# Optimization experiments

Hardware: AMD Instinct MI355X
Metric: run time of the kernel (lower is better)

## Reference

```python
import jax, jax.numpy as jnp
import numpy as np

jax.config.update("jax_enable_x64", True)  # anchor_ids * 2654435761 needs int64, matching torch semantics

B, NV, D = 200000, 5, 64
CANTOR_DEPTH = 8
VOLUME_SCALE = 10.0
VOLUME_W, EDGE_W, SPREAD_W = 0.4, 0.3, 0.3
EPS = 1e-6
KNUTH = 2654435761


def setup_inputs() -> dict:
    key = jax.random.key(0)
    vertices = jax.random.normal(key, (B, NV, D), dtype=jnp.float32)
    anchor_ids = jnp.arange(B, dtype=jnp.int64)
    return {"vertices": vertices, "anchor_ids": anchor_ids}


def reference(vertices, anchor_ids):
    dtype = vertices.dtype
    b = vertices.shape[0]

    # pairwise squared distances between the 5 vertices: [B, 5, 5]
    diff = vertices[:, :, None, :] - vertices[:, None, :, :]
    dist_sq = (diff ** 2).sum(-1)

    # Cayley-Menger 6x6 matrix and 4-simplex volume
    M = jnp.zeros((b, 6, 6), dtype=dtype)
    M = M.at[:, 0, 1:].set(1.0)
    M = M.at[:, 1:, 0].set(1.0)
    M = M.at[:, 1:, 1:].set(dist_sq)
    det = jnp.linalg.det(M)
    volume = jnp.sqrt(jnp.clip(-det / 9216.0, 0.0))

    # edge statistics over the 10 unique edges (unbiased std, as torch.std)
    iu, ju = np.triu_indices(5, k=1)
    edges = jnp.sqrt(dist_sq[:, iu, ju])  # [B, 10]
    mean_edge = edges.mean(axis=1)
    std_edge = edges.std(axis=1, ddof=1)

    # vertex spread: std of distances to centroid (unbiased)
    centroid = vertices.mean(axis=1, keepdims=True)
    dists = jnp.linalg.norm(vertices - centroid, axis=-1)  # [B, 5]
    spread = dists.std(axis=1, ddof=1)

    volume_norm = jax.nn.sigmoid(volume * VOLUME_SCALE)
    edge_ratio = jax.nn.sigmoid(std_edge / (mean_edge + EPS))
    spread_norm = jax.nn.sigmoid(spread)
    seed = volume_norm * VOLUME_W + edge_ratio * EDGE_W + spread_norm * SPREAD_W

    # anchor id hash contribution (int64 modular arithmetic as in torch)
    id_contrib = ((anchor_ids.astype(jnp.int64) * KNUTH) % 1000000).astype(dtype) / 1000000.0
    seed = 0.1 * seed + 0.9 * id_contrib
    seed = jnp.clip(seed, EPS, 1.0 - EPS)

    # Cantor digit extraction (unrolled fixed-depth loop)
    x = seed
    cantor_val = jnp.zeros_like(x)
    factor = 0.5
    for _ in range(CANTOR_DEPTH):
        x_scaled = x * 3.0
        digit = x_scaled.astype(jnp.int32)  # trunc == floor for x >= 0
        x = x_scaled - digit.astype(dtype)
        cantor_val = cantor_val + (digit == 2).astype(dtype) * factor
        factor *= 0.5
    return jnp.clip(cantor_val, 0.0, 1.0)
```

## Files before the change

### kernel.cpp

```cpp
#include <hip/hip_runtime.h>
#include <stdint.h>


#define THREADS 256
#define ANCH_PER_BLOCK 256

__global__ __launch_bounds__(THREADS) void fingerprint_kernel(
    const float* __restrict__ vertices,
    const void* __restrict__ ids_raw,
    float* __restrict__ out,
    int n)
{
    __shared__ double stats[ANCH_PER_BLOCK][17];

    const int tid  = threadIdx.x;
    const int wave = tid >> 6;
    const int lane = tid & 63;
    const int g    = lane >> 4;
    const int r    = lane & 15;
    const int blockBase = blockIdx.x * ANCH_PER_BLOCK;

    const int PI[10] = {0,0,0,0,1,1,1,2,2,3};
    const int PJ[10] = {1,2,3,4,2,3,4,3,4,4};

    #pragma unroll 1
    for (int it = 0; it < ANCH_PER_BLOCK / (4 * 4); ++it) {
        const int alocal = wave * 64 + it * 4 + g;
        int a = blockBase + alocal;
        int aload = (a < n) ? a : (n - 1);

        const float4* vp = (const float4*)(vertices + (size_t)aload * 320);
        float xv[5][4];
        #pragma unroll
        for (int v = 0; v < 5; ++v) {
            float4 t = vp[v * 16 + r];
            xv[v][0] = t.x; xv[v][1] = t.y; xv[v][2] = t.z; xv[v][3] = t.w;
        }

        double ds[10], sd[5];
        #pragma unroll
        for (int p = 0; p < 10; ++p) ds[p] = 0.0;
        #pragma unroll
        for (int v = 0; v < 5; ++v) sd[v] = 0.0;

        #pragma unroll
        for (int k = 0; k < 4; ++k) {
            double x0 = (double)xv[0][k], x1 = (double)xv[1][k],
                   x2 = (double)xv[2][k], x3 = (double)xv[3][k],
                   x4 = (double)xv[4][k];
            double c = (x0 + x1 + x2 + x3 + x4) * 0.2;
            double d0 = x0 - c, d1 = x1 - c, d2 = x2 - c, d3 = x3 - c, d4 = x4 - c;
            sd[0] += d0 * d0; sd[1] += d1 * d1; sd[2] += d2 * d2;
            sd[3] += d3 * d3; sd[4] += d4 * d4;
            double xs[5] = {x0, x1, x2, x3, x4};
            #pragma unroll
            for (int p = 0; p < 10; ++p) {
                double dd = xs[PI[p]] - xs[PJ[p]];
                ds[p] += dd * dd;
            }
        }

        #pragma unroll
        for (int p = 0; p < 10; ++p) {
            ds[p] += __shfl_xor(ds[p], 1);
            ds[p] += __shfl_xor(ds[p], 2);
            ds[p] += __shfl_xor(ds[p], 4);
            ds[p] += __shfl_xor(ds[p], 8);
        }
        #pragma unroll
        for (int v = 0; v < 5; ++v) {
            sd[v] += __shfl_xor(sd[v], 1);
            sd[v] += __shfl_xor(sd[v], 2);
            sd[v] += __shfl_xor(sd[v], 4);
            sd[v] += __shfl_xor(sd[v], 8);
        }

        if (r < 10)       stats[alocal][r]      = ds[r];
        else if (r < 15)  stats[alocal][r]      = sd[r - 10];
    }

    __syncthreads();

    const int a = blockBase + tid;
    if (a >= n) return;

    double ds[10], sd[5];
    #pragma unroll
    for (int p = 0; p < 10; ++p) ds[p] = stats[tid][p];
    #pragma unroll
    for (int v = 0; v < 5; ++v) sd[v] = stats[tid][10 + v];

    const int PIDX[5][5] = {
        {-1, 0, 1, 2, 3},
        { 0,-1, 4, 5, 6},
        { 1, 4,-1, 7, 8},
        { 2, 5, 7,-1, 9},
        { 3, 6, 8, 9,-1}};

    double M[6][6];
    M[0][0] = 0.0;
    #pragma unroll
    for (int j = 1; j < 6; ++j) { M[0][j] = 1.0; M[j][0] = 1.0; }
    #pragma unroll
    for (int i = 0; i < 5; ++i)
        #pragma unroll
        for (int j = 0; j < 5; ++j)
            M[1 + i][1 + j] = (i == j) ? 0.0 : ds[PIDX[i][j]];

    double sign = 1.0;
    #pragma unroll
    for (int k = 0; k < 6; ++k) {
        #pragma unroll
        for (int i = k + 1; i < 6; ++i) {
            bool sw = fabs(M[i][k]) > fabs(M[k][k]);
            #pragma unroll
            for (int j = 0; j < 6; ++j) {
                double tk = M[k][j], ti = M[i][j];
                M[k][j] = sw ? ti : tk;
                M[i][j] = sw ? tk : ti;
            }
            sign = sw ? -sign : sign;
        }
        double rp = 1.0 / M[k][k];
        #pragma unroll
        for (int i = k + 1; i < 6; ++i) {
            double l = M[i][k] * rp;
            #pragma unroll
            for (int j = k + 1; j < 6; ++j)
                M[i][j] -= l * M[k][j];
        }
    }
    double det = sign;
    #pragma unroll
    for (int k = 0; k < 6; ++k) det *= M[k][k];

    double volume = sqrt(fmax(-det / 9216.0, 0.0));

    double e[10], esum = 0.0;
    #pragma unroll
    for (int p = 0; p < 10; ++p) { e[p] = sqrt(ds[p]); esum += e[p]; }
    double emean = esum * 0.1;
    double evar = 0.0;
    #pragma unroll
    for (int p = 0; p < 10; ++p) { double d = e[p] - emean; evar += d * d; }
    double estd = sqrt(evar / 9.0);

    double dd[5], dsum = 0.0;
    #pragma unroll
    for (int v = 0; v < 5; ++v) { dd[v] = sqrt(sd[v]); dsum += dd[v]; }
    double dmean = dsum * 0.2;
    double svar = 0.0;
    #pragma unroll
    for (int v = 0; v < 5; ++v) { double d = dd[v] - dmean; svar += d * d; }
    double spread = sqrt(svar * 0.25);

    double vn = 1.0 / (1.0 + exp(-10.0 * volume));
    double er = 1.0 / (1.0 + exp(-(estd / (emean + 1e-6))));
    double sn = 1.0 / (1.0 + exp(-spread));
    double seed = 0.4 * vn + 0.3 * er + 0.3 * sn;

    const int* ai32 = (const int*)ids_raw;
    long long idv;
    if (ai32[1] == 0) {
        idv = ((const long long*)ids_raw)[a];
    } else {
        idv = (long long)ai32[a];
    }
    long long h = (idv * 2654435761LL) % 1000000LL;
    double idc = (double)h / 1000000.0;

    seed = 0.1 * seed + 0.9 * idc;
    seed = fmin(fmax(seed, 1e-6), 1.0 - 1e-6);

    double x = seed, cant = 0.0, factor = 0.5;
    #pragma unroll
    for (int itc = 0; itc < 8; ++itc) {
        double xs = x * 3.0;
        int dg = (int)xs;
        x = xs - (double)dg;
        cant += (dg == 2) ? factor : 0.0;
        factor *= 0.5;
    }
    out[a] = (float)fmin(fmax(cant, 0.0), 1.0);
}

extern "C" void kernel_launch(void* const* d_in, const int* in_sizes, int n_in,
                              void* d_out, int out_size, void* d_ws, size_t ws_size,
                              hipStream_t stream) {
    const float* vertices = (const float*)d_in[0];
    const void*  ids      = d_in[1];
    float* out = (float*)d_out;
    int n = in_sizes[1];
    int grid = (n + ANCH_PER_BLOCK - 1) / ANCH_PER_BLOCK;
    fingerprint_kernel<<<grid, THREADS, 0, stream>>>(vertices, ids, out, n);
}
```

Measured before the change: 379.9 us.

## Compute Gram inner products and replace Cayley-Menger LU with Gram determinant

Phase one now accumulates the 15 pairwise inner products per anchor in fp64, using 8 lanes per anchor with two float4 loads each. Pairwise distances, centroid distances and a 4x4 Gram matrix are derived from these products, and the volume comes from a closed-form Gram determinant instead of a pivoted 6x6 LU. This trims FP64 work, shuffle rounds and the heavy elimination code. It risks cancellation error when distances are recovered from inner products.

```diff
diff --git a/kernel.cpp b/kernel.cpp
--- a/kernel.cpp
+++ b/kernel.cpp
@@ -16,67 +16,67 @@
     const int tid  = threadIdx.x;
     const int wave = tid >> 6;
     const int lane = tid & 63;
-    const int g    = lane >> 4;
-    const int r    = lane & 15;
+    const int g    = lane >> 3;
+    const int r    = lane & 7;
     const int blockBase = blockIdx.x * ANCH_PER_BLOCK;
 
-    const int PI[10] = {0,0,0,0,1,1,1,2,2,3};
-    const int PJ[10] = {1,2,3,4,2,3,4,3,4,4};
-
-    #pragma unroll 1
-    for (int it = 0; it < ANCH_PER_BLOCK / (4 * 4); ++it) {
-        const int alocal = wave * 64 + it * 4 + g;
+    #pragma unroll 2
+    for (int it = 0; it < 8; ++it) {
+        const int alocal = wave * 64 + it * 8 + g;
         int a = blockBase + alocal;
         int aload = (a < n) ? a : (n - 1);
 
         const float4* vp = (const float4*)(vertices + (size_t)aload * 320);
-        float xv[5][4];
+        float xa[5][4], xb[5][4];
         #pragma unroll
         for (int v = 0; v < 5; ++v) {
             float4 t = vp[v * 16 + r];
-            xv[v][0] = t.x; xv[v][1] = t.y; xv[v][2] = t.z; xv[v][3] = t.w;
-        }
-
-        double ds[10], sd[5];
-        #pragma unroll
-        for (int p = 0; p < 10; ++p) ds[p] = 0.0;
-        #pragma unroll
-        for (int v = 0; v < 5; ++v) sd[v] = 0.0;
+            xa[v][0] = t.x; xa[v][1] = t.y; xa[v][2] = t.z; xa[v][3] = t.w;
+        }
+        #pragma unroll
+        for (int v = 0; v < 5; ++v) {
+            float4 t = vp[v * 16 + 8 + r];
+            xb[v][0] = t.x; xb[v][1] = t.y; xb[v][2] = t.z; xb[v][3] = t.w;
+        }
+
+        double ip[15];
+        #pragma unroll
+        for (int p = 0; p < 15; ++p) ip[p] = 0.0;
 
         #pragma unroll
         for (int k = 0; k < 4; ++k) {
-            double x0 = (double)xv[0][k], x1 = (double)xv[1][k],
-                   x2 = (double)xv[2][k], x3 = (double)xv[3][k],
-                   x4 = (double)xv[4][k];
-            double c = (x0 + x1 + x2 + x3 + x4) * 0.2;
-            double d0 = x0 - c, d1 = x1 - c, d2 = x2 - c, d3 = x3 - c, d4 = x4 - c;
-            sd[0] += d0 * d0; sd[1] += d1 * d1; sd[2] += d2 * d2;
-            sd[3] += d3 * d3; sd[4] += d4 * d4;
-            double xs[5] = {x0, x1, x2, x3, x4};
-            #pragma unroll
-            for (int p = 0; p < 10; ++p) {
-                double dd = xs[PI[p]] - xs[PJ[p]];
-                ds[p] += dd * dd;
-            }
-        }
-
-        #pragma unroll
-        for (int p = 0; p < 10; ++p) {
-            ds[p] += __shfl_xor(ds[p], 1);
-            ds[p] += __shfl_xor(ds[p], 2);
-            ds[p] += __shfl_xor(ds[p], 4);
-            ds[p] += __shfl_xor(ds[p], 8);
-        }
-        #pragma unroll
-        for (int v = 0; v < 5; ++v) {
-            sd[v] += __shfl_xor(sd[v], 1);
-            sd[v] += __shfl_xor(sd[v], 2);
-            sd[v] += __shfl_xor(sd[v], 4);
-            sd[v] += __shfl_xor(sd[v], 8);
-        }
-
-        if (r < 10)       stats[alocal][r]      = ds[r];
-        else if (r < 15)  stats[alocal][r]      = sd[r - 10];
+            double x[5];
+            #pragma unroll
+            for (int v = 0; v < 5; ++v) x[v] = (double)xa[v][k];
+            int p = 0;
+            #pragma unroll
+            for (int v = 0; v < 5; ++v)
+                #pragma unroll
+                for (int w = v; w < 5; ++w)
+                    ip[p++] = fma(x[v], x[w], ip[p]);
+        }
+        #pragma unroll
+        for (int k = 0; k < 4; ++k) {
+            double x[5];
+            #pragma unroll
+            for (int v = 0; v < 5; ++v) x[v] = (double)xb[v][k];
+            int p = 0;
+            #pragma unroll
+            for (int v = 0; v < 5; ++v)
+                #pragma unroll
+                for (int w = v; w < 5; ++w)
+                    ip[p++] = fma(x[v], x[w], ip[p]);
+        }
+
+        #pragma unroll
+        for (int p = 0; p < 15; ++p) {
+            ip[p] += __shfl_xor(ip[p], 1);
+            ip[p] += __shfl_xor(ip[p], 2);
+            ip[p] += __shfl_xor(ip[p], 4);
+        }
+
+        stats[alocal][r] = ip[r];
+        if (r < 7) stats[alocal][8 + r] = ip[8 + r];
     }
 
     __syncthreads();
@@ -84,75 +84,85 @@
     const int a = blockBase + tid;
     if (a >= n) return;
 
-    double ds[10], sd[5];
-    #pragma unroll
-    for (int p = 0; p < 10; ++p) ds[p] = stats[tid][p];
-    #pragma unroll
-    for (int v = 0; v < 5; ++v) sd[v] = stats[tid][10 + v];
-
-    const int PIDX[5][5] = {
-        {-1, 0, 1, 2, 3},
-        { 0,-1, 4, 5, 6},
-        { 1, 4,-1, 7, 8},
-        { 2, 5, 7,-1, 9},
-        { 3, 6, 8, 9,-1}};
-
-    double M[6][6];
-    M[0][0] = 0.0;
-    #pragma unroll
-    for (int j = 1; j < 6; ++j) { M[0][j] = 1.0; M[j][0] = 1.0; }
-    #pragma unroll
-    for (int i = 0; i < 5; ++i)
-        #pragma unroll
-        for (int j = 0; j < 5; ++j)
-            M[1 + i][1 + j] = (i == j) ? 0.0 : ds[PIDX[i][j]];
-
-    double sign = 1.0;
-    #pragma unroll
-    for (int k = 0; k < 6; ++k) {
-        #pragma unroll
-        for (int i = k + 1; i < 6; ++i) {
-            bool sw = fabs(M[i][k]) > fabs(M[k][k]);
-            #pragma unroll
-            for (int j = 0; j < 6; ++j) {
-                double tk = M[k][j], ti = M[i][j];
-                M[k][j] = sw ? ti : tk;
-                M[i][j] = sw ? tk : ti;
+    double ip[15];
+    #pragma unroll
+    for (int p = 0; p < 15; ++p) ip[p] = stats[tid][p];
+
+    const int IP[5][5] = {
+        { 0, 1, 2, 3, 4},
+        { 1, 5, 6, 7, 8},
+        { 2, 6, 9,10,11},
+        { 3, 7,10,12,13},
+        { 4, 8,11,13,14}};
+
+    double dsq[5][5];
+    #pragma unroll
+    for (int i = 0; i < 5; ++i) {
+        dsq[i][i] = 0.0;
+        #pragma unroll
+        for (int j = i + 1; j < 5; ++j) {
+            double d = ip[IP[i][i]] + ip[IP[j][j]] - 2.0 * ip[IP[i][j]];
+            dsq[i][j] = d; dsq[j][i] = d;
+        }
+    }
+
+    double esum = 0.0, e[10];
+    {
+        int p = 0;
+        #pragma unroll
+        for (int i = 0; i < 5; ++i)
+            #pragma unroll
+            for (int j = i + 1; j < 5; ++j) {
+                e[p] = sqrt(dsq[i][j]); esum += e[p]; ++p;
             }
-            sign = sw ? -sign : sign;
-        }
-        double rp = 1.0 / M[k][k];
-        #pragma unroll
-        for (int i = k + 1; i < 6; ++i) {
-            double l = M[i][k] * rp;
-            #pragma unroll
-            for (int j = k + 1; j < 6; ++j)
-                M[i][j] -= l * M[k][j];
-        }
-    }
-    double det = sign;
-    #pragma unroll
-    for (int k = 0; k < 6; ++k) det *= M[k][k];
-
-    double volume = sqrt(fmax(-det / 9216.0, 0.0));
-
-    double e[10], esum = 0.0;
-    #pragma unroll
-    for (int p = 0; p < 10; ++p) { e[p] = sqrt(ds[p]); esum += e[p]; }
+    }
     double emean = esum * 0.1;
     double evar = 0.0;
     #pragma unroll
     for (int p = 0; p < 10; ++p) { double d = e[p] - emean; evar += d * d; }
     double estd = sqrt(evar / 9.0);
 
-    double dd[5], dsum = 0.0;
-    #pragma unroll
-    for (int v = 0; v < 5; ++v) { dd[v] = sqrt(sd[v]); dsum += dd[v]; }
+    double rowsum[5], tot = 0.0;
+    #pragma unroll
+    for (int i = 0; i < 5; ++i) {
+        double s = 0.0;
+        #pragma unroll
+        for (int w = 0; w < 5; ++w) s += ip[IP[i][w]];
+        rowsum[i] = s; tot += s;
+    }
+    double c2 = tot * 0.04;
+    double dsum = 0.0, dd[5];
+    #pragma unroll
+    for (int i = 0; i < 5; ++i) {
+        double s2 = ip[IP[i][i]] - 0.4 * rowsum[i] + c2;
+        dd[i] = sqrt(fmax(s2, 0.0)); dsum += dd[i];
+    }
     double dmean = dsum * 0.2;
     double svar = 0.0;
     #pragma unroll
-    for (int v = 0; v < 5; ++v) { double d = dd[v] - dmean; svar += d * d; }
+    for (int i = 0; i < 5; ++i) { double d = dd[i] - dmean; svar += d * d; }
     double spread = sqrt(svar * 0.25);
+
+    double G[4][4];
+    #pragma unroll
+    for (int i = 0; i < 4; ++i)
+        #pragma unroll
+        for (int j = 0; j < 4; ++j)
+            G[i][j] = 0.5 * (dsq[0][i + 1] + dsq[0][j + 1] - dsq[i + 1][j + 1]);
+
+    double m01 = G[2][2] * G[3][3] - G[2][3] * G[3][2];
+    double m02 = G[2][1] * G[3][3] - G[2][3] * G[3][1];
+    double m03 = G[2][1] * G[3][2] - G[2][2] * G[3][1];
+    double m04 = G[2][0] * G[3][3] - G[2][3] * G[3][0];
+    double m05 = G[2][0] * G[3][2] - G[2][2] * G[3][0];
+    double m06 = G[2][0] * G[3][1] - G[2][1] * G[3][0];
+    double det =
+        G[0][0] * (G[1][1] * m01 - G[1][2] * m02 + G[1][3] * m03)
+      - G[0][1] * (G[1][0] * m01 - G[1][2] * m04 + G[1][3] * m05)
+      + G[0][2] * (G[1][0] * m02 - G[1][1] * m04 + G[1][3] * m06)
+      - G[0][3] * (G[1][0] * m03 - G[1][1] * m05 + G[1][2] * m06);
+
+    double volume = sqrt(fmax(det / 576.0, 0.0));
 
     double vn = 1.0 / (1.0 + exp(-10.0 * volume));
     double er = 1.0 / (1.0 + exp(-(estd / (emean + 1e-6))));
```

After: 353.9 us. -6.9%, faster.
